# Kernel optimization log

Measured on AMD Instinct MI355X. Metric: run time of the kernel, lower is better.

The kernel has to match this reference:

```python
import jax, jax.numpy as jnp
import numpy as np

NUM_QUBITS = 6
DIM = 2 ** NUM_QUBITS  # 64


def _u_gate(theta, phi, lam):
    # qiskit U(theta, phi, lam)
    c = jnp.cos(theta / 2).astype(jnp.complex64)
    s = jnp.sin(theta / 2).astype(jnp.complex64)
    ephi = jnp.exp(1j * phi.astype(jnp.complex64))
    elam = jnp.exp(1j * lam.astype(jnp.complex64))
    return jnp.stack([
        jnp.stack([c, -elam * s]),
        jnp.stack([ephi * s, ephi * elam * c]),
    ])


def _p_gate(lam):
    one = jnp.ones((), jnp.complex64)
    return jnp.stack([
        jnp.stack([one, jnp.zeros((), jnp.complex64)]),
        jnp.stack([jnp.zeros((), jnp.complex64), jnp.exp(1j * lam.astype(jnp.complex64))]),
    ])


def _controlled(U):
    # 4x4 matrix in |control, target> basis: block-diag(I2, U)
    return jnp.eye(4, dtype=jnp.complex64).at[2:, 2:].set(U)


_CX = jnp.array([[1, 0, 0, 0], [0, 1, 0, 0], [0, 0, 0, 1], [0, 0, 1, 0]], dtype=jnp.complex64)


def _apply_1q(psi, U, q):
    # psi: (B, 2,2,2,2,2,2); qubit q (qiskit little-endian) -> axis 6-q
    ax = NUM_QUBITS - q
    psi = jnp.moveaxis(psi, ax, -1)
    psi = psi @ U.T
    return jnp.moveaxis(psi, -1, ax)


def _apply_2q(psi, G, qa, qb):
    # G is 4x4 acting on (qa, qb) with index 2*bit(qa)+bit(qb)
    a, b = NUM_QUBITS - qa, NUM_QUBITS - qb
    psi = jnp.moveaxis(psi, (a, b), (-2, -1))
    shp = psi.shape
    psi = (psi.reshape(shp[:-2] + (4,)) @ G.T).reshape(shp)
    return jnp.moveaxis(psi, (-2, -1), (a, b))


def _circuit(features, params):
    # amplitude encoding (qc.initialize with L2 normalization; |0> fallback for zero vec)
    norm = jnp.linalg.norm(features, axis=1, keepdims=True)
    safe = jnp.where(jnp.isclose(norm, 0.0), 1.0, norm)
    e0 = jnp.zeros((1, DIM), features.dtype).at[0, 0].set(1.0)
    psi = jnp.where(jnp.isclose(norm, 0.0), e0, features / safe)
    psi = psi.astype(jnp.complex64).reshape((-1,) + (2,) * NUM_QUBITS)

    def U3(i):
        return _u_gate(params[i], params[i + 1], params[i + 2])

    # layer 1: U on all qubits (params 0..17)
    for q in range(NUM_QUBITS):
        psi = _apply_1q(psi, U3(3 * q), q)
    # cx(2,1); p(18,1); cx(4,3); p(19,3)
    psi = _apply_2q(psi, _CX, 2, 1)
    psi = _apply_1q(psi, _p_gate(params[18]), 1)
    psi = _apply_2q(psi, _CX, 4, 3)
    psi = _apply_1q(psi, _p_gate(params[19]), 3)
    # layer 2: U on [0,1,3,5] (params 20..31)
    idx = 20
    for q in [0, 1, 3, 5]:
        psi = _apply_1q(psi, U3(idx), q)
        idx += 3
    # controlled-U(32..34) ctrl 0 -> tgt 1; controlled-U(35..37) ctrl 3 -> tgt 5
    psi = _apply_2q(psi, _controlled(U3(32)), 0, 1)
    psi = _apply_2q(psi, _controlled(U3(35)), 3, 5)
    # cx(3,1); p(38,1)
    psi = _apply_2q(psi, _CX, 3, 1)
    psi = _apply_1q(psi, _p_gate(params[38]), 1)
    # final: U on [0,1] (39..44); CU(45..47) ctrl 0 -> tgt 1; U on [0,1] (48..53)
    psi = _apply_1q(psi, U3(39), 0)
    psi = _apply_1q(psi, U3(42), 1)
    psi = _apply_2q(psi, _controlled(U3(45)), 0, 1)
    psi = _apply_1q(psi, U3(48), 0)
    psi = _apply_1q(psi, U3(51), 1)

    # observable kron(diag(1,-1), I_32): +1 for index < 32, -1 otherwise (Z on qubit 5)
    probs = jnp.abs(psi.reshape(-1, DIM)) ** 2
    sign = jnp.where(jnp.arange(DIM) < DIM // 2, 1.0, -1.0).astype(jnp.float32)
    return (probs @ sign).astype(jnp.float32)


def setup_inputs() -> dict:
    key = jax.random.key(0)
    kf, kp = jax.random.split(key)
    features = jax.random.normal(kf, (262144, 64), dtype=jnp.float32)
    params = jax.random.uniform(kp, (54,), dtype=jnp.float32) * (0.1 * np.pi)
    return {"features": features, "params": params}


def reference(features, params):
    return _circuit(features, params)
```

## Files before the change

### kernel.cpp

```cpp
#include <hip/hip_runtime.h>

using f32x4  = __attribute__((ext_vector_type(4))) float;
using bf16x8 = __attribute__((ext_vector_type(8))) short;

__device__ inline unsigned short f2bf(float x) {
  unsigned u = __builtin_bit_cast(unsigned, x);
  return (unsigned short)((u + 0x7FFFu + ((u >> 16) & 1u)) >> 16);
}
__device__ inline float2 cmul(float2 a, float2 b) {
  return make_float2(a.x * b.x - a.y * b.y, a.x * b.y + a.y * b.x);
}
__device__ inline float2 cadd(float2 a, float2 b) { return make_float2(a.x + b.x, a.y + b.y); }

__device__ inline void gate1q(float2* psi, int t, int sub, int q,
                              float2 u00, float2 u01, float2 u10, float2 u11) {
  const int bit = 1 << q, mask = bit - 1;
#pragma unroll
  for (int pp = 0; pp < 8; ++pp) {
    int p  = sub * 8 + pp;
    int i0 = ((p & ~mask) << 1) | (p & mask);
    int i1 = i0 | bit;
    float2 a0 = psi[i0 * 64 + t], a1 = psi[i1 * 64 + t];
    psi[i0 * 64 + t] = cadd(cmul(u00, a0), cmul(u01, a1));
    psi[i1 * 64 + t] = cadd(cmul(u10, a0), cmul(u11, a1));
  }
}

__device__ inline void gatec(float2* psi, int t, int sub, int c, int g,
                             float2 v00, float2 v01, float2 v10, float2 v11) {
  const int cb = 1 << c, gb = 1 << g;
  const int lo = (c < g ? c : g), hi = (c < g ? g : c);
  const int mlo = (1 << lo) - 1, mhi = (1 << hi) - 1;
#pragma unroll
  for (int pp = 0; pp < 4; ++pp) {
    int p = sub * 4 + pp;
    int y = ((p & ~mlo) << 1) | (p & mlo);
    y     = ((y & ~mhi) << 1) | (y & mhi);
    int i0 = y | cb;
    int i1 = i0 | gb;
    float2 a0 = psi[i0 * 64 + t], a1 = psi[i1 * 64 + t];
    psi[i0 * 64 + t] = cadd(cmul(v00, a0), cmul(v01, a1));
    psi[i1 * 64 + t] = cadd(cmul(v10, a0), cmul(v11, a1));
  }
}

#define MFMA(A, B, C) __builtin_amdgcn_mfma_f32_16x16x32_bf16(A, B, C, 0, 0, 0)

__global__ __launch_bounds__(256) void qfused(const float* __restrict__ F,
                                              const float* __restrict__ Pp,
                                              float* __restrict__ out) {
  __shared__ float2 psi[64 * 64];
  __shared__ __attribute__((aligned(16))) unsigned short Plds[128 * 64];
  __shared__ float tS[54], tC[54], tSh[54], tCh[54];
  __shared__ float sA00;

  const int tid = threadIdx.x;
  const int t = tid & 63, sub = tid >> 6;

  if (tid < 54) {
    float p = Pp[tid];
    tS[tid]  = __sinf(p);
    tC[tid]  = __cosf(p);
    tSh[tid] = __sinf(0.5f * p);
    tCh[tid] = __cosf(0.5f * p);
  }
  for (int idx = tid; idx < 4096; idx += 256)
    psi[idx] = make_float2(((idx >> 6) == (idx & 63)) ? 1.f : 0.f, 0.f);
  __syncthreads();

  float2 u00, u01, u10, u11;
  const float2 Z = make_float2(0.f, 0.f), ONE = make_float2(1.f, 0.f);
  auto U3L = [&](int i) {
    float ch = tCh[i], sh = tSh[i];
    float cp = tC[i + 1], sp = tS[i + 1];
    float cl = tC[i + 2], sl = tS[i + 2];
    u00 = make_float2(ch, 0.f);
    u01 = make_float2(-cl * sh, -sl * sh);
    u10 = make_float2(cp * sh, sp * sh);
    u11 = make_float2((cp * cl - sp * sl) * ch, (cp * sl + sp * cl) * ch);
  };
  auto PH = [&](int i) { return make_float2(tC[i], tS[i]); };

#pragma unroll
  for (int q = 0; q < 6; ++q) {
    U3L(3 * q); gate1q(psi, t, sub, q, u00, u01, u10, u11); __syncthreads();
  }
  gatec(psi, t, sub, 2, 1, Z, ONE, ONE, Z); __syncthreads();
  gate1q(psi, t, sub, 1, ONE, Z, Z, PH(18)); __syncthreads();
  gatec(psi, t, sub, 4, 3, Z, ONE, ONE, Z); __syncthreads();
  gate1q(psi, t, sub, 3, ONE, Z, Z, PH(19)); __syncthreads();
  const int qs[4] = {0, 1, 3, 5};
#pragma unroll
  for (int ii = 0; ii < 4; ++ii) {
    U3L(20 + 3 * ii); gate1q(psi, t, sub, qs[ii], u00, u01, u10, u11); __syncthreads();
  }
  U3L(32); gatec(psi, t, sub, 0, 1, u00, u01, u10, u11); __syncthreads();
  U3L(35); gatec(psi, t, sub, 3, 5, u00, u01, u10, u11); __syncthreads();
  gatec(psi, t, sub, 3, 1, Z, ONE, ONE, Z); __syncthreads();
  gate1q(psi, t, sub, 1, ONE, Z, Z, PH(38)); __syncthreads();
  U3L(39); gate1q(psi, t, sub, 0, u00, u01, u10, u11); __syncthreads();
  U3L(42); gate1q(psi, t, sub, 1, u00, u01, u10, u11); __syncthreads();
  U3L(45); gatec(psi, t, sub, 0, 1, u00, u01, u10, u11); __syncthreads();
  U3L(48); gate1q(psi, t, sub, 0, u00, u01, u10, u11); __syncthreads();
  U3L(51); gate1q(psi, t, sub, 1, u00, u01, u10, u11); __syncthreads();

  if (tid < 64) {
    float2 v = psi[tid * 64];
    float term = (v.x * v.x + v.y * v.y) * (tid < 32 ? 1.f : -1.f);
#pragma unroll
    for (int m = 1; m < 64; m <<= 1) term += __shfl_xor(term, m, 64);
    if (tid == 0) sA00 = term;
  }
  for (int idx = tid; idx < 8192; idx += 256) {
    int r = idx >> 6, j = idx & 63;
    int i = (r < 32) ? r : (r < 96) ? (r - 32) : (r - 64);
    bool im = (r >= 32 && r < 64) || (r >= 96);
    float2 v = psi[i * 64 + j];
    Plds[idx] = f2bf(im ? v.y : v.x);
  }
  __syncthreads();

  const int lane = tid & 63, wid = sub;
  const int g = lane >> 4, c0 = lane & 15;
  const unsigned short* pb = Plds + c0 * 64 + g * 8;
  bf16x8 Bf[8][2];
#pragma unroll
  for (int nt = 0; nt < 8; ++nt) {
    Bf[nt][0] = *(const bf16x8*)(pb + nt * 1024);
    Bf[nt][1] = *(const bf16x8*)(pb + nt * 1024 + 32);
  }
  const float A00 = sA00;

  const int tile0 = blockIdx.x * 64 + wid * 16;
  const float* fp = F + (size_t)(tile0 * 16 + c0) * 64 + g * 8;

#define LOADT(i, V0, V1, V2, V3) { const float* q_ = fp + (size_t)(i) * 1024; \
    V0 = *(const float4*)(q_); V1 = *(const float4*)(q_ + 4); \
    V2 = *(const float4*)(q_ + 32); V3 = *(const float4*)(q_ + 36); }

#define PROCESS(i, V0, V1, V2, V3) { \
    bf16x8 a0, a1; \
    a0[0] = f2bf(V0.x); a0[1] = f2bf(V0.y); a0[2] = f2bf(V0.z); a0[3] = f2bf(V0.w); \
    a0[4] = f2bf(V1.x); a0[5] = f2bf(V1.y); a0[6] = f2bf(V1.z); a0[7] = f2bf(V1.w); \
    a1[0] = f2bf(V2.x); a1[1] = f2bf(V2.y); a1[2] = f2bf(V2.z); a1[3] = f2bf(V2.w); \
    a1[4] = f2bf(V3.x); a1[5] = f2bf(V3.y); a1[6] = f2bf(V3.z); a1[7] = f2bf(V3.w); \
    f32x4 acc[8]; \
    _Pragma("unroll") \
    for (int nt = 0; nt < 8; ++nt) { \
      acc[nt] = (f32x4){0.f, 0.f, 0.f, 0.f}; \
      acc[nt] = MFMA(a0, Bf[nt][0], acc[nt]); \
      acc[nt] = MFMA(a1, Bf[nt][1], acc[nt]); \
    } \
    float s1[4] = {0, 0, 0, 0}, s2[4] = {0, 0, 0, 0}; \
    _Pragma("unroll") \
    for (int nt = 0; nt < 4; ++nt) { \
      _Pragma("unroll") \
      for (int r = 0; r < 4; ++r) { \
        s1[r] = fmaf(acc[nt][r], acc[nt][r], s1[r]); \
        s2[r] = fmaf(acc[nt + 4][r], acc[nt + 4][r], s2[r]); \
      } \
    } \
    _Pragma("unroll") \
    for (int m = 1; m < 16; m <<= 1) { \
      _Pragma("unroll") \
      for (int r = 0; r < 4; ++r) { \
        s1[r] += __shfl_xor(s1[r], m, 64); \
        s2[r] += __shfl_xor(s2[r], m, 64); \
      } \
    } \
    if (c0 < 4) { \
      float sp_ = (c0 == 0) ? s1[0] : (c0 == 1) ? s1[1] : (c0 == 2) ? s1[2] : s1[3]; \
      float sm_ = (c0 == 0) ? s2[0] : (c0 == 1) ? s2[1] : (c0 == 2) ? s2[2] : s2[3]; \
      float den = sp_ + sm_; \
      out[(size_t)(tile0 + (i)) * 16 + 4 * g + c0] = (den < 1e-30f) ? A00 : (sp_ - sm_) / den; \
    } }

  float4 x0, x1, x2, x3, y0, y1, y2, y3;
  LOADT(0, x0, x1, x2, x3);
#pragma unroll
  for (int i = 0; i < 16; i += 2) {
    LOADT(i + 1, y0, y1, y2, y3);
    PROCESS(i, x0, x1, x2, x3);
    if (i + 2 < 16) LOADT(i + 2, x0, x1, x2, x3);
    PROCESS(i + 1, y0, y1, y2, y3);
  }
#undef LOADT
#undef PROCESS
}

extern "C" void kernel_launch(void* const* d_in, const int* in_sizes, int n_in,
                              void* d_out, int out_size, void* d_ws, size_t ws_size,
                              hipStream_t stream) {
  const float* F = (const float*)d_in[0];
  const float* P = (const float*)d_in[1];
  float* out = (float*)d_out;
  qfused<<<256, 256, 0, stream>>>(F, P, out);
}
```

Before: 120.0 us.

## Spread row tiles over 768 blocks and transpose MFMA operands to simplify reduction

The grid is tripled to 768 blocks, and each wave now handles 5 or 6 tiles of 16 rows (16384 tiles balanced over 3072 waves) instead of 16, with launch bounds asking for 3 blocks per CU. The MFMA operand order is swapped so rows map to output columns, which cuts the per-tile reduction to two cross-lane shuffles. The aim is more waves in flight to hide global-memory latency and a cheaper epilogue. In exchange, each block redoes the 64x64 unitary construction in LDS, and three times as many blocks pay that fixed setup cost.

```diff
diff --git a/kernel.cpp b/kernel.cpp
--- a/kernel.cpp
+++ b/kernel.cpp
@@ -46,9 +46,9 @@
 
 #define MFMA(A, B, C) __builtin_amdgcn_mfma_f32_16x16x32_bf16(A, B, C, 0, 0, 0)
 
-__global__ __launch_bounds__(256) void qfused(const float* __restrict__ F,
-                                              const float* __restrict__ Pp,
-                                              float* __restrict__ out) {
+__global__ __launch_bounds__(256, 3) void qfused(const float* __restrict__ F,
+                                                 const float* __restrict__ Pp,
+                                                 float* __restrict__ out) {
   __shared__ float2 psi[64 * 64];
   __shared__ __attribute__((aligned(16))) unsigned short Plds[128 * 64];
   __shared__ float tS[54], tC[54], tSh[54], tCh[54];
@@ -125,14 +125,16 @@
   const unsigned short* pb = Plds + c0 * 64 + g * 8;
   bf16x8 Bf[8][2];
 #pragma unroll
-  for (int nt = 0; nt < 8; ++nt) {
-    Bf[nt][0] = *(const bf16x8*)(pb + nt * 1024);
-    Bf[nt][1] = *(const bf16x8*)(pb + nt * 1024 + 32);
+  for (int mt = 0; mt < 8; ++mt) {
+    Bf[mt][0] = *(const bf16x8*)(pb + mt * 1024);
+    Bf[mt][1] = *(const bf16x8*)(pb + mt * 1024 + 32);
   }
   const float A00 = sA00;
 
-  const int tile0 = blockIdx.x * 64 + wid * 16;
-  const float* fp = F + (size_t)(tile0 * 16 + c0) * 64 + g * 8;
+  const int gid   = (int)blockIdx.x * 4 + wid;
+  const int start = gid * 5 + (gid < 1024 ? gid : 1024);
+  const int count = 5 + (gid < 1024 ? 1 : 0);
+  const float* fp = F + (size_t)start * 1024 + (size_t)c0 * 64 + g * 8;
 
 #define LOADT(i, V0, V1, V2, V3) { const float* q_ = fp + (size_t)(i) * 1024; \
     V0 = *(const float4*)(q_); V1 = *(const float4*)(q_ + 4); \
@@ -146,43 +148,37 @@
     a1[4] = f2bf(V3.x); a1[5] = f2bf(V3.y); a1[6] = f2bf(V3.z); a1[7] = f2bf(V3.w); \
     f32x4 acc[8]; \
     _Pragma("unroll") \
-    for (int nt = 0; nt < 8; ++nt) { \
-      acc[nt] = (f32x4){0.f, 0.f, 0.f, 0.f}; \
-      acc[nt] = MFMA(a0, Bf[nt][0], acc[nt]); \
-      acc[nt] = MFMA(a1, Bf[nt][1], acc[nt]); \
+    for (int mt = 0; mt < 8; ++mt) { \
+      acc[mt] = (f32x4){0.f, 0.f, 0.f, 0.f}; \
+      acc[mt] = MFMA(Bf[mt][0], a0, acc[mt]); \
+      acc[mt] = MFMA(Bf[mt][1], a1, acc[mt]); \
     } \
-    float s1[4] = {0, 0, 0, 0}, s2[4] = {0, 0, 0, 0}; \
+    float sp_ = 0.f, sm_ = 0.f; \
     _Pragma("unroll") \
-    for (int nt = 0; nt < 4; ++nt) { \
+    for (int mt = 0; mt < 4; ++mt) { \
       _Pragma("unroll") \
       for (int r = 0; r < 4; ++r) { \
-        s1[r] = fmaf(acc[nt][r], acc[nt][r], s1[r]); \
-        s2[r] = fmaf(acc[nt + 4][r], acc[nt + 4][r], s2[r]); \
+        sp_ = fmaf(acc[mt][r], acc[mt][r], sp_); \
+        sm_ = fmaf(acc[mt + 4][r], acc[mt + 4][r], sm_); \
       } \
     } \
-    _Pragma("unroll") \
-    for (int m = 1; m < 16; m <<= 1) { \
-      _Pragma("unroll") \
-      for (int r = 0; r < 4; ++r) { \
-        s1[r] += __shfl_xor(s1[r], m, 64); \
-        s2[r] += __shfl_xor(s2[r], m, 64); \
-      } \
-    } \
-    if (c0 < 4) { \
-      float sp_ = (c0 == 0) ? s1[0] : (c0 == 1) ? s1[1] : (c0 == 2) ? s1[2] : s1[3]; \
-      float sm_ = (c0 == 0) ? s2[0] : (c0 == 1) ? s2[1] : (c0 == 2) ? s2[2] : s2[3]; \
+    sp_ += __shfl_xor(sp_, 16, 64); sm_ += __shfl_xor(sm_, 16, 64); \
+    sp_ += __shfl_xor(sp_, 32, 64); sm_ += __shfl_xor(sm_, 32, 64); \
+    if (lane < 16) { \
       float den = sp_ + sm_; \
-      out[(size_t)(tile0 + (i)) * 16 + 4 * g + c0] = (den < 1e-30f) ? A00 : (sp_ - sm_) / den; \
+      out[(size_t)(start + (i)) * 16 + c0] = (den < 1e-30f) ? A00 : (sp_ - sm_) / den; \
     } }
 
   float4 x0, x1, x2, x3, y0, y1, y2, y3;
   LOADT(0, x0, x1, x2, x3);
 #pragma unroll
-  for (int i = 0; i < 16; i += 2) {
-    LOADT(i + 1, y0, y1, y2, y3);
+  for (int i = 0; i < 6; i += 2) {
+    if (i >= count) break;
+    const bool has2 = (i + 1 < count);
+    if (has2) LOADT(i + 1, y0, y1, y2, y3);
     PROCESS(i, x0, x1, x2, x3);
-    if (i + 2 < 16) LOADT(i + 2, x0, x1, x2, x3);
-    PROCESS(i + 1, y0, y1, y2, y3);
+    if (i + 2 < count) LOADT(i + 2, x0, x1, x2, x3);
+    if (has2) PROCESS(i + 1, y0, y1, y2, y3);
   }
 #undef LOADT
 #undef PROCESS
@@ -194,5 +190,5 @@
   const float* F = (const float*)d_in[0];
   const float* P = (const float*)d_in[1];
   float* out = (float*)d_out;
-  qfused<<<256, 256, 0, stream>>>(F, P, out);
+  qfused<<<768, 256, 0, stream>>>(F, P, out);
 }
```

After: 114.3 us. 4.8% less time.
